# Performance work log

Measured on AMD Instinct MI355X. Metric: run time of the kernel, lower is better.

The kernel has to match this reference:

```python
import jax, jax.numpy as jnp
import numpy as np

THRESH = 0.5
DECAY = 0.2
D_IN = 784
H1 = 2048
H2 = 10
K = 10
U = D_IN + H1
L = 128
B = 1024


def setup_inputs() -> dict:
    key = jax.random.key(0)
    ks = jax.random.split(key, 6)
    inp = jax.random.uniform(ks[0], (B, D_IN), dtype=jnp.float32)
    W1 = jax.random.normal(ks[1], (H1, D_IN), dtype=jnp.float32) * 0.05
    b1 = jnp.zeros((H1,), dtype=jnp.float32)
    W2 = jax.random.normal(ks[2], (H2, H1), dtype=jnp.float32) * 0.05
    b2 = jnp.zeros((H2,), dtype=jnp.float32)
    # core_mem_all[k][u][0] -> sparse-ish per-unit vector, [1] -> count
    core_mem_vec = (jax.random.uniform(ks[3], (K, U, L)) > 0.7).astype(jnp.float32)
    core_mem_cnt = jax.random.randint(ks[4], (K, U), 0, 5).astype(jnp.int32)
    return {"input": inp, "W1": W1, "b1": b1, "W2": W2, "b2": b2,
            "core_mem_vec": core_mem_vec, "core_mem_cnt": core_mem_cnt,
            "time_window": 20}


def act_fun(mem):
    # spike = Heaviside(mem - thresh)
    return (mem > THRESH).astype(mem.dtype)


def reference(input, W1, b1, W2, b2, core_mem_vec, core_mem_cnt, time_window):
    batch, d_in = input.shape
    h1 = W1.shape[0]
    h2 = W2.shape[0]
    Lv = core_mem_vec.shape[-1]

    # Precompute, per (core k, unit u): contribution to count_add_1 / count_add_2
    # when unit u spikes. count_add_1 += (last nonzero index of temp) - 1 when cnt>0;
    # count_add_2 += cnt when cnt>0. Sum over cores up front (loop order irrelevant).
    nz = core_mem_vec != 0                                     # [K,U,L]
    has = nz.any(-1)
    last_idx = Lv - 1 - jnp.argmax(nz[..., ::-1].astype(jnp.int32), axis=-1)  # [K,U]
    active = (core_mem_cnt > 0) & has
    val1 = jnp.where(active, last_idx - 1, 0).sum(0).astype(jnp.float32)      # [U]
    val2 = jnp.where(core_mem_cnt > 0, core_mem_cnt, 0).sum(0).astype(jnp.float32)
    v1x, v1h = val1[:d_in], val1[d_in:]
    v2x, v2h = val2[:d_in], val2[d_in:]

    key = jax.random.key(42)

    def step(carry, t):
        h1m, h1s, h2m, h2s, h2sum, a1, a2, cs = carry
        # Bernoulli rate encoding of the input image
        x = (input > jax.random.uniform(jax.random.fold_in(key, t), input.shape)).astype(jnp.float32)
        # mem_update: mem = mem*decay*(1-spike) + W x + b ; spike = mem > thresh
        h1m = h1m * DECAY * (1.0 - h1s) + x @ W1.T + b1
        h1s = act_fun(h1m)
        h2m = h2m * DECAY * (1.0 - h2s) + h1s @ W2.T + b2
        h2s = act_fun(h2m)
        h2sum = h2sum + h2s
        # vectorized core-memory gather/count: sum per-unit precomputed values
        # over all spiking units, across the batch
        xs = x.sum(0)      # [784] spike counts per input unit this step
        hs = h1s.sum(0)    # [h1]
        a1 = a1 + xs @ v1x + hs @ v1h
        a2 = a2 + xs @ v2x + hs @ v2h
        cs = cs + xs.sum() + hs.sum()
        return (h1m, h1s, h2m, h2s, h2sum, a1, a2, cs), None

    z1 = jnp.zeros((batch, h1), dtype=jnp.float32)
    z2 = jnp.zeros((batch, h2), dtype=jnp.float32)
    carry = (z1, z1, z2, z2, z2, jnp.float32(0), jnp.float32(0), jnp.float32(0))
    carry, _ = jax.lax.scan(step, carry, jnp.arange(time_window))
    _, _, _, _, h2sum, a1, a2, cs = carry
    outputs = h2sum / time_window
    return outputs, a1, a2, cs
```

## Files before the change

### kernel.cpp

```cpp
#include <hip/hip_runtime.h>
#include <cstdint>
#include <cstddef>

static constexpr int D_IN = 784;
static constexpr int H1   = 2048;
static constexpr int H2   = 10;
static constexpr int KK   = 10;
static constexpr int UU   = 2832;
static constexpr int LL   = 128;
static constexpr int BB   = 1024;
static constexpr int TT   = 20;
static constexpr int HALF = BB * D_IN / 2;
static constexpr int NCH  = 25;
static constexpr int NLIMB = 3;
static constexpr int XA_T  = 32 * NCH * 64;
static constexpr int BITS_T = BB * 64;
static constexpr int PANEL = NCH * NLIMB * 64;
static constexpr int NPART_GEN = 2000;
static constexpr int NPART_H1  = 256;
static constexpr int NPART = NPART_GEN + NPART_H1;

static constexpr int BLK_VALS  = UU / 4;
static constexpr int BLK_W2T   = H1 / 256;
static constexpr int BLK_LIMBS = (64 * NCH * 64) / 256;
static constexpr int BLK_TRANS = D_IN * 4;
static constexpr int SETUP_BLOCKS = BLK_VALS + BLK_W2T + BLK_LIMBS + BLK_TRANS;

typedef int v4i  __attribute__((ext_vector_type(4)));
typedef int v16i __attribute__((ext_vector_type(16)));

#define MFMA_I8 __builtin_amdgcn_mfma_i32_32x32x32_i8

__device__ __forceinline__ uint32_t rotl32(uint32_t x, int d) {
  return (x << d) | (x >> (32 - d));
}
__device__ __forceinline__ void threefry2x32(uint32_t k0, uint32_t k1,
                                             uint32_t& x0, uint32_t& x1) {
  uint32_t ks2 = k0 ^ k1 ^ 0x1BD11BDAu;
  x0 += k0; x1 += k1;
#define TF_R(r) { x0 += x1; x1 = rotl32(x1, (r)); x1 ^= x0; }
  TF_R(13) TF_R(15) TF_R(26) TF_R(6)
  x0 += k1;  x1 += ks2 + 1u;
  TF_R(17) TF_R(29) TF_R(16) TF_R(24)
  x0 += ks2; x1 += k0 + 2u;
  TF_R(13) TF_R(15) TF_R(26) TF_R(6)
  x0 += k0;  x1 += k1 + 3u;
  TF_R(17) TF_R(29) TF_R(16) TF_R(24)
  x0 += k1;  x1 += ks2 + 4u;
  TF_R(13) TF_R(15) TF_R(26) TF_R(6)
  x0 += ks2; x1 += k0 + 5u;
#undef TF_R
}
__device__ __forceinline__ float bits_to_unif(uint32_t b) {
  uint32_t fb = (b >> 9) | 0x3F800000u;
  return __uint_as_float(fb) - 1.0f;
}

__device__ __forceinline__ double wave_red(double v) {
  #pragma unroll
  for (int off = 32; off > 0; off >>= 1) v += __shfl_down(v, off, 64);
  return v;
}
__device__ __forceinline__ void block_store3(double s0, double s1, double s2,
                                             double* slot) {
  __shared__ double lds[3][8];
  int lane = threadIdx.x & 63, w = threadIdx.x >> 6;
  int nw = (int)(blockDim.x >> 6);
  s0 = wave_red(s0); s1 = wave_red(s1); s2 = wave_red(s2);
  if (lane == 0) { lds[0][w] = s0; lds[1][w] = s1; lds[2][w] = s2; }
  __syncthreads();
  if (threadIdx.x == 0) {
    double t0 = 0, t1 = 0, t2 = 0;
    for (int i = 0; i < nw; i++) { t0 += lds[0][i]; t1 += lds[1][i]; t2 += lds[2][i]; }
    slot[0] = t0; slot[1] = t1; slot[2] = t2;
  }
}

__global__ __launch_bounds__(256)
void setup(const float* __restrict__ cmv, const int* __restrict__ cmc,
           float* __restrict__ v1, float* __restrict__ v2,
           const float* __restrict__ W2, float* __restrict__ W2T,
           const float* __restrict__ W1, v4i* __restrict__ W1L,
           const float* __restrict__ input, float* __restrict__ inT) {
  int bx = blockIdx.x;
  if (bx < BLK_VALS) {
    int u = bx * 4 + (threadIdx.x >> 6);
    int lane = threadIdx.x & 63;
    float acc1 = 0.0f, acc2 = 0.0f;
    for (int k = 0; k < KK; k++) {
      const float* p = cmv + ((size_t)k * UU + u) * LL;
      float a = p[lane];
      float b = p[lane + 64];
      unsigned long long mlo = __ballot(a != 0.0f);
      unsigned long long mhi = __ballot(b != 0.0f);
      int c = cmc[k * UU + u];
      if (c > 0) {
        int last = mhi ? (127 - __builtin_clzll(mhi))
                       : (mlo ? (63 - __builtin_clzll(mlo)) : -1);
        if (last >= 0) acc1 += (float)(last - 1);
        acc2 += (float)c;
      }
    }
    if (lane == 0) { v1[u] = acc1; v2[u] = acc2; }
  } else if (bx < BLK_VALS + BLK_W2T) {
    int i = (bx - BLK_VALS) * 256 + threadIdx.x;
    #pragma unroll
    for (int j = 0; j < H2; j++) W2T[i * H2 + j] = W2[j * H1 + i];
  } else if (bx < BLK_VALS + BLK_W2T + BLK_LIMBS) {
    int tid = (bx - BLK_VALS - BLK_W2T) * 256 + threadIdx.x;
    int lane = tid & 63;
    int tc = tid >> 6;
    int n = ((tc / NCH) << 5) + (lane & 31);
    int chunk = tc % NCH;
    int k0 = chunk * 32 + (lane >> 5) * 16;
    union { v4i v; signed char b[16]; } d[NLIMB];
    #pragma unroll
    for (int j = 0; j < 16; j++) {
      long long F = 0;
      int k = k0 + j;
      if (k < D_IN) {
        double w = (double)W1[(size_t)n * D_IN + k];
        F = llround(w * 0x1p24);
        if (F >  8355711LL) F =  8355711LL;
        if (F < -8421504LL) F = -8421504LL;
      }
      #pragma unroll
      for (int l = 0; l < NLIMB; l++) {
        int dig = (int)((F + 128) & 255) - 128;
        d[l].b[j] = (signed char)dig;
        F = (F - dig) >> 8;
      }
    }
    #pragma unroll
    for (int l = 0; l < NLIMB; l++) W1L[(size_t)(tc * NLIMB + l) * 64 + lane] = d[l].v;
  } else {
    int b = bx - (BLK_VALS + BLK_W2T + BLK_LIMBS);
    int k = b >> 2;
    int m = ((b & 3) << 8) + threadIdx.x;
    inT[(size_t)k * BB + m] = input[(size_t)m * D_IN + k];
  }
}

__global__ __launch_bounds__(256)
void gen_all(const float* __restrict__ inT, v4i* __restrict__ XA,
             const float* __restrict__ v1, const float* __restrict__ v2,
             double* __restrict__ gpart) {
  int t  = blockIdx.x / 100;
  int gw = (blockIdx.x % 100) * 4 + (threadIdx.x >> 6);
  int lane = threadIdx.x & 63;
  int mtile = gw / NCH, chunk = gw - mtile * NCH;
  int m = (mtile << 5) + (lane & 31);
  int k0 = chunk * 32 + (lane >> 5) * 16;
  uint32_t f0 = 0u, f1 = (uint32_t)t;
  threefry2x32(0u, 42u, f0, f1);
  union { v4i v; unsigned char b[16]; } r0, r1;
  double s0 = 0, s1 = 0, s2 = 0;
  v4i* XA_t = XA + (size_t)t * XA_T;
  if (k0 < D_IN) {
    #pragma unroll
    for (int j = 0; j < 16; j++) {
      int k = k0 + j;
      uint32_t c0 = (uint32_t)(m * D_IN + k), c1 = c0 + (uint32_t)HALF;
      threefry2x32(f0, f1, c0, c1);
      float u0 = bits_to_unif(c0), u1 = bits_to_unif(c1);
      float i0 = inT[(size_t)k * BB + m];
      float i1 = inT[(size_t)k * BB + m + 512];
      unsigned char x0 = (i0 > u0) ? 1 : 0;
      unsigned char x1 = (i1 > u1) ? 1 : 0;
      r0.b[j] = x0; r1.b[j] = x1;
      double xsum = (double)(x0 + x1);
      s0 += xsum * (double)v1[k];
      s1 += xsum * (double)v2[k];
      s2 += xsum;
    }
  } else {
    r0.v = (v4i){0, 0, 0, 0};
    r1.v = (v4i){0, 0, 0, 0};
  }
  XA_t[(size_t)(mtile * NCH + chunk) * 64 + lane] = r0.v;
  XA_t[(size_t)((mtile + 16) * NCH + chunk) * 64 + lane] = r1.v;
  block_store3(s0, s1, s2, gpart + 3 * (size_t)blockIdx.x);
}

__global__ __launch_bounds__(512, 2)
void h1_all(const v4i* __restrict__ XA, const v4i* __restrict__ W1L,
            const float* __restrict__ b1, uint32_t* __restrict__ bits,
            const float* __restrict__ v1, const float* __restrict__ v2,
            double* __restrict__ gpart) {
  extern __shared__ v4i bl[];
  int lane = threadIdx.x & 63, wv = threadIdx.x >> 6;
  int id = blockIdx.x + (blockIdx.y << 6);
  int xcd = id & 7;
  int idx = id >> 3;
  int ntile = (idx << 1) | (xcd >> 2);
  int mtg = xcd & 3;
  int mt = mtg * 8 + wv;
  {
    const v4i* wp = W1L + (size_t)ntile * PANEL;
    for (int i = threadIdx.x; i < PANEL; i += 512) bl[i] = wp[i];
  }
  __syncthreads();

  int col = lane & 31;
  int gn = (ntile << 5) + col;
  float bias = b1[gn];
  double v1n = (double)v1[D_IN + gn], v2n = (double)v2[D_IN + gn];
  int scnt = 0;
  float mreg[16];
  #pragma unroll
  for (int r = 0; r < 16; r++) mreg[r] = 0.0f;

  const v4i* bq = bl + lane;
  v4i B00 = bq[0],   B01 = bq[64],  B02 = bq[128];
  v4i B10 = bq[192], B11 = bq[256], B12 = bq[320];
  const v4i* a0 = XA + (size_t)mt * (NCH * 64) + lane;
  const v4i* a1 = a0 + XA_T;
  v4i A00 = a0[0], A10 = a1[0], A01 = a0[64], A11 = a1[64];

  #pragma unroll 1
  for (int tp = 0; tp < TT / 2; tp++) {
    v16i c00 = {}, c01 = {}, c02 = {};
    v16i c10 = {}, c11 = {}, c12 = {};
    __builtin_amdgcn_s_setprio(1);
    c00 = MFMA_I8(A00, B00, c00, 0, 0, 0);
    c10 = MFMA_I8(A10, B00, c10, 0, 0, 0);
    c01 = MFMA_I8(A00, B01, c01, 0, 0, 0);
    c11 = MFMA_I8(A10, B01, c11, 0, 0, 0);
    c02 = MFMA_I8(A00, B02, c02, 0, 0, 0);
    c12 = MFMA_I8(A10, B02, c12, 0, 0, 0);
    c00 = MFMA_I8(A01, B10, c00, 0, 0, 0);
    c10 = MFMA_I8(A11, B10, c10, 0, 0, 0);
    c01 = MFMA_I8(A01, B11, c01, 0, 0, 0);
    c11 = MFMA_I8(A11, B11, c11, 0, 0, 0);
    c02 = MFMA_I8(A01, B12, c02, 0, 0, 0);
    c12 = MFMA_I8(A11, B12, c12, 0, 0, 0);
    #pragma unroll
    for (int c = 2; c < NCH; c++) {
      v4i A0 = a0[c * 64], A1 = a1[c * 64];
      const v4i* br = bq + (size_t)c * (NLIMB * 64);
      v4i B0 = br[0], B1 = br[64], B2 = br[128];
      c00 = MFMA_I8(A0, B0, c00, 0, 0, 0);
      c10 = MFMA_I8(A1, B0, c10, 0, 0, 0);
      c01 = MFMA_I8(A0, B1, c01, 0, 0, 0);
      c11 = MFMA_I8(A1, B1, c11, 0, 0, 0);
      c02 = MFMA_I8(A0, B2, c02, 0, 0, 0);
      c12 = MFMA_I8(A1, B2, c12, 0, 0, 0);
    }
    __builtin_amdgcn_s_setprio(0);
    {
      const v4i* a0n = a0 + ((tp + 1 < TT / 2) ? 2 * XA_T : 0);
      const v4i* a1n = a0n + XA_T;
      A00 = a0n[0]; A10 = a1n[0]; A01 = a0n[64]; A11 = a1n[64];
      a0 = a0n; a1 = a1n;
    }
    #pragma unroll
    for (int half = 0; half < 2; half++) {
      const v16i& q0 = half ? c10 : c00;
      const v16i& q1 = half ? c11 : c01;
      const v16i& q2 = half ? c12 : c02;
      uint32_t* btm = bits + (size_t)(2 * tp + half) * BITS_T
                    + ((size_t)mt << 5) * 64 + ntile;
      #pragma unroll
      for (int r = 0; r < 16; r++) {
        int val = (int)((uint32_t)q0[r] + ((uint32_t)q1[r] << 8)
                        + ((uint32_t)q2[r] << 16));
        float dot = (float)val * 0x1p-24f + bias;
        float mp = mreg[r];
        float mnew = (mp > 0.5f) ? dot : fmaf(mp, 0.2f, dot);
        bool s = (mnew > 0.5f);
        mreg[r] = mnew;
        unsigned long long bm = __ballot(s);
        int rowA = (r & 3) + 8 * (r >> 2);
        if ((lane & 31) == 0)
          btm[(size_t)(rowA + ((lane >> 5) << 2)) * 64] = (uint32_t)(bm >> (lane & 32));
        scnt += s ? 1 : 0;
      }
    }
  }
  double sc = (double)scnt;
  block_store3(sc * v1n, sc * v2n, sc, gpart + 3 * (size_t)(NPART_GEN + id));
}

__global__ __launch_bounds__(256)
void h2_all(const uint32_t* __restrict__ bits, const float* __restrict__ W2T,
            const float* __restrict__ b2, const double* __restrict__ gpart,
            float* __restrict__ out) {
  int lane = threadIdx.x & 63, wq = threadIdx.x >> 6;
  int b0 = blockIdx.x * 2;
  float w[8][10];
  #pragma unroll
  for (int c = 0; c < 8; c++) {
    int n = (wq << 9) + (c << 6) + lane;
    #pragma unroll
    for (int j = 0; j < 10; j++) w[c][j] = W2T[(size_t)n * H2 + j];
  }
  float m = 0.0f, sp = 0.0f, sm = 0.0f;
  float b2v = (lane < 10) ? b2[lane] : 0.0f;
  __shared__ float part[4][2][10];
  #pragma unroll 1
  for (int t = 0; t < TT; t++) {
    const uint32_t* bt = bits + (size_t)t * BITS_T;
    #pragma unroll
    for (int r = 0; r < 2; r++) {
      uint32_t myw = bt[(size_t)(b0 + r) * 64 + (wq << 4) + (lane & 15)];
      float p[10];
      #pragma unroll
      for (int j = 0; j < 10; j++) p[j] = 0.0f;
      #pragma unroll
      for (int c = 0; c < 8; c++) {
        uint32_t wd = __shfl(myw, (c << 1) + (lane >> 5), 64);
        float f = (float)((wd >> (lane & 31)) & 1u);
        #pragma unroll
        for (int j = 0; j < 10; j++) p[j] += f * w[c][j];
      }
      #pragma unroll
      for (int j = 0; j < 10; j++) {
        float v = p[j];
        #pragma unroll
        for (int off = 32; off > 0; off >>= 1) v += __shfl_xor(v, off, 64);
        p[j] = v;
      }
      if (lane == 0) {
        #pragma unroll
        for (int j = 0; j < 10; j++) part[wq][r][j] = p[j];
      }
    }
    __syncthreads();
    if (wq < 2 && lane < 10) {
      float red = part[0][wq][lane] + part[1][wq][lane]
                + part[2][wq][lane] + part[3][wq][lane];
      m = m * 0.2f * (1.0f - sp) + red + b2v;
      sp = (m > 0.5f) ? 1.0f : 0.0f;
      sm += sp;
    }
    __syncthreads();
  }
  if (wq < 2 && lane < 10)
    out[(size_t)(b0 + wq) * H2 + lane] = (float)((double)sm / (double)TT);

  if (blockIdx.x == 0) {
    double t0 = 0, t1 = 0, t2 = 0;
    for (int i = threadIdx.x; i < NPART; i += 256) {
      t0 += gpart[3 * (size_t)i];
      t1 += gpart[3 * (size_t)i + 1];
      t2 += gpart[3 * (size_t)i + 2];
    }
    __shared__ double fin[3][4];
    t0 = wave_red(t0); t1 = wave_red(t1); t2 = wave_red(t2);
    if (lane == 0) { fin[0][wq] = t0; fin[1][wq] = t1; fin[2][wq] = t2; }
    __syncthreads();
    if (threadIdx.x == 0) {
      double a = 0, b = 0, cc = 0;
      #pragma unroll
      for (int i = 0; i < 4; i++) { a += fin[0][i]; b += fin[1][i]; cc += fin[2][i]; }
      out[(size_t)BB * H2 + 0] = (float)a;
      out[(size_t)BB * H2 + 1] = (float)b;
      out[(size_t)BB * H2 + 2] = (float)cc;
    }
  }
}

extern "C" void kernel_launch(void* const* d_in, const int* in_sizes, int n_in,
                              void* d_out, int out_size, void* d_ws, size_t ws_size,
                              hipStream_t stream) {
  (void)in_sizes; (void)n_in; (void)out_size; (void)ws_size;
  const float* input = (const float*)d_in[0];
  const float* W1    = (const float*)d_in[1];
  const float* b1    = (const float*)d_in[2];
  const float* W2    = (const float*)d_in[3];
  const float* b2    = (const float*)d_in[4];
  const float* cmv   = (const float*)d_in[5];
  const int*   cmc   = (const int*)d_in[6];

  char* base = (char*)d_ws;
  float*  v1   = (float*)(base + 0);
  float*  v2   = (float*)(base + 11328);
  float*  W2T  = (float*)(base + 22656);
  v4i*    W1L  = (v4i*)(base + 104576);
  v4i*    XA   = (v4i*)(base + 5019776);
  uint32_t* bits = (uint32_t*)(base + 21403776);
  float*  inT  = (float*)(base + 26646656);
  double* gpart = (double*)(base + 29857920);

  setup<<<SETUP_BLOCKS, 256, 0, stream>>>(cmv, cmc, v1, v2, W2, W2T, W1, W1L,
                                          input, inT);
  gen_all<<<TT * 100, 256, 0, stream>>>(inT, XA, v1, v2, gpart);
  h1_all<<<dim3(64, 4), 512, PANEL * 16, stream>>>(XA, W1L, b1, bits, v1, v2,
                                                   gpart);
  h2_all<<<BB / 2, 256, 0, stream>>>(bits, W2T, b2, gpart, (float*)d_out);
}
```

Measured before the change: 285.8 us.

## Fuse all four stages into one cooperative persistent kernel with grid syncs

Replaces the four separate launches (setup, Bernoulli generation, int8-MFMA hidden layer, output layer) with one cooperative kernel of 256 blocks of 512 threads, separated by grid-wide barriers. Each block handles two virtual 256-thread blocks in the setup and generation phases. This removes launch gaps and kernel-boundary drains. The h1 phase also preloads a third B/A chunk and staggers odd waves with s_sleep, and the h2 phase is remapped to 4 rows per block. The cost is that the setup and generation phases now run on only 256 resident blocks, and grid.sync adds barrier overhead.

```diff
diff --git a/kernel.cpp b/kernel.cpp
--- a/kernel.cpp
+++ b/kernel.cpp
@@ -1,4 +1,5 @@
 #include <hip/hip_runtime.h>
+#include <hip/hip_cooperative_groups.h>
 #include <cstdint>
 #include <cstddef>
 
@@ -25,6 +26,7 @@
 static constexpr int BLK_LIMBS = (64 * NCH * 64) / 256;
 static constexpr int BLK_TRANS = D_IN * 4;
 static constexpr int SETUP_BLOCKS = BLK_VALS + BLK_W2T + BLK_LIMBS + BLK_TRANS;
+static constexpr int BLK_GEN   = TT * 100;
 
 typedef int v4i  __attribute__((ext_vector_type(4)));
 typedef int v16i __attribute__((ext_vector_type(16)));
@@ -61,301 +63,340 @@
   for (int off = 32; off > 0; off >>= 1) v += __shfl_down(v, off, 64);
   return v;
 }
+__device__ __forceinline__ void half_store3(double s0, double s1, double s2,
+                                            double* slot, bool act) {
+  __shared__ double hl[2][3][4];
+  int h = threadIdx.x >> 8, lane = threadIdx.x & 63, w = (threadIdx.x >> 6) & 3;
+  s0 = wave_red(s0); s1 = wave_red(s1); s2 = wave_red(s2);
+  if (lane == 0) { hl[h][0][w] = s0; hl[h][1][w] = s1; hl[h][2][w] = s2; }
+  __syncthreads();
+  if ((threadIdx.x & 255) == 0 && act) {
+    double t0 = 0, t1 = 0, t2 = 0;
+    #pragma unroll
+    for (int i = 0; i < 4; i++) { t0 += hl[h][0][i]; t1 += hl[h][1][i]; t2 += hl[h][2][i]; }
+    slot[0] = t0; slot[1] = t1; slot[2] = t2;
+  }
+  __syncthreads();
+}
 __device__ __forceinline__ void block_store3(double s0, double s1, double s2,
                                              double* slot) {
   __shared__ double lds[3][8];
   int lane = threadIdx.x & 63, w = threadIdx.x >> 6;
-  int nw = (int)(blockDim.x >> 6);
   s0 = wave_red(s0); s1 = wave_red(s1); s2 = wave_red(s2);
   if (lane == 0) { lds[0][w] = s0; lds[1][w] = s1; lds[2][w] = s2; }
   __syncthreads();
   if (threadIdx.x == 0) {
     double t0 = 0, t1 = 0, t2 = 0;
-    for (int i = 0; i < nw; i++) { t0 += lds[0][i]; t1 += lds[1][i]; t2 += lds[2][i]; }
+    #pragma unroll
+    for (int i = 0; i < 8; i++) { t0 += lds[0][i]; t1 += lds[1][i]; t2 += lds[2][i]; }
     slot[0] = t0; slot[1] = t1; slot[2] = t2;
   }
 }
 
-__global__ __launch_bounds__(256)
-void setup(const float* __restrict__ cmv, const int* __restrict__ cmc,
-           float* __restrict__ v1, float* __restrict__ v2,
-           const float* __restrict__ W2, float* __restrict__ W2T,
-           const float* __restrict__ W1, v4i* __restrict__ W1L,
-           const float* __restrict__ input, float* __restrict__ inT) {
-  int bx = blockIdx.x;
-  if (bx < BLK_VALS) {
-    int u = bx * 4 + (threadIdx.x >> 6);
-    int lane = threadIdx.x & 63;
-    float acc1 = 0.0f, acc2 = 0.0f;
-    for (int k = 0; k < KK; k++) {
-      const float* p = cmv + ((size_t)k * UU + u) * LL;
-      float a = p[lane];
-      float b = p[lane + 64];
-      unsigned long long mlo = __ballot(a != 0.0f);
-      unsigned long long mhi = __ballot(b != 0.0f);
-      int c = cmc[k * UU + u];
-      if (c > 0) {
-        int last = mhi ? (127 - __builtin_clzll(mhi))
-                       : (mlo ? (63 - __builtin_clzll(mlo)) : -1);
-        if (last >= 0) acc1 += (float)(last - 1);
-        acc2 += (float)c;
-      }
-    }
-    if (lane == 0) { v1[u] = acc1; v2[u] = acc2; }
-  } else if (bx < BLK_VALS + BLK_W2T) {
-    int i = (bx - BLK_VALS) * 256 + threadIdx.x;
+__global__ __launch_bounds__(512, 2)
+void scnn_all(const float* __restrict__ cmv, const int* __restrict__ cmc,
+              float* __restrict__ v1, float* __restrict__ v2,
+              const float* __restrict__ W2, float* __restrict__ W2T,
+              const float* __restrict__ W1, v4i* __restrict__ W1L,
+              const float* __restrict__ input, float* __restrict__ inT,
+              v4i* __restrict__ XA, const float* __restrict__ b1,
+              uint32_t* __restrict__ bits, double* __restrict__ gpart,
+              const float* __restrict__ b2, float* __restrict__ out) {
+  namespace cg = cooperative_groups;
+  cg::grid_group grid = cg::this_grid();
+  extern __shared__ v4i bl[];
+  int tid = threadIdx.x, bid = blockIdx.x;
+
+  for (int it = 0; it < (SETUP_BLOCKS + 511) / 512; ++it) {
+    int vb = it * 512 + bid * 2 + (tid >> 8);
+    int vt = tid & 255;
+    if (vb >= SETUP_BLOCKS) continue;
+    if (vb < BLK_VALS) {
+      int u = vb * 4 + (vt >> 6);
+      int lane = vt & 63;
+      float acc1 = 0.0f, acc2 = 0.0f;
+      for (int k = 0; k < KK; k++) {
+        const float* p = cmv + ((size_t)k * UU + u) * LL;
+        float a = p[lane];
+        float b = p[lane + 64];
+        unsigned long long mlo = __ballot(a != 0.0f);
+        unsigned long long mhi = __ballot(b != 0.0f);
+        int c = cmc[k * UU + u];
+        if (c > 0) {
+          int last = mhi ? (127 - __builtin_clzll(mhi))
+                         : (mlo ? (63 - __builtin_clzll(mlo)) : -1);
+          if (last >= 0) acc1 += (float)(last - 1);
+          acc2 += (float)c;
+        }
+      }
+      if (lane == 0) { v1[u] = acc1; v2[u] = acc2; }
+    } else if (vb < BLK_VALS + BLK_W2T) {
+      int i = (vb - BLK_VALS) * 256 + vt;
+      #pragma unroll
+      for (int j = 0; j < H2; j++) W2T[i * H2 + j] = W2[j * H1 + i];
+    } else if (vb < BLK_VALS + BLK_W2T + BLK_LIMBS) {
+      int tl = (vb - BLK_VALS - BLK_W2T) * 256 + vt;
+      int lane = tl & 63;
+      int tc = tl >> 6;
+      int n = ((tc / NCH) << 5) + (lane & 31);
+      int chunk = tc % NCH;
+      int k0 = chunk * 32 + (lane >> 5) * 16;
+      union { v4i v; signed char b[16]; } d[NLIMB];
+      #pragma unroll
+      for (int j = 0; j < 16; j++) {
+        long long F = 0;
+        int k = k0 + j;
+        if (k < D_IN) {
+          double w = (double)W1[(size_t)n * D_IN + k];
+          F = llround(w * 0x1p24);
+          if (F >  8355711LL) F =  8355711LL;
+          if (F < -8421504LL) F = -8421504LL;
+        }
+        #pragma unroll
+        for (int l = 0; l < NLIMB; l++) {
+          int dig = (int)((F + 128) & 255) - 128;
+          d[l].b[j] = (signed char)dig;
+          F = (F - dig) >> 8;
+        }
+      }
+      #pragma unroll
+      for (int l = 0; l < NLIMB; l++) W1L[(size_t)(tc * NLIMB + l) * 64 + lane] = d[l].v;
+    } else {
+      int b = vb - (BLK_VALS + BLK_W2T + BLK_LIMBS);
+      int k = b >> 2;
+      int m = ((b & 3) << 8) + vt;
+      inT[(size_t)k * BB + m] = input[(size_t)m * D_IN + k];
+    }
+  }
+  grid.sync();
+
+  for (int it = 0; it < (BLK_GEN + 511) / 512; ++it) {
+    int vb = it * 512 + bid * 2 + (tid >> 8);
+    int vt = tid & 255;
+    bool act = (vb < BLK_GEN);
+    double s0 = 0, s1 = 0, s2 = 0;
+    if (act) {
+      int lane = vt & 63;
+      int t = vb / 100;
+      int gw = (vb % 100) * 4 + (vt >> 6);
+      int mtile = gw / NCH, chunk = gw - mtile * NCH;
+      int m = (mtile << 5) + (lane & 31);
+      int k0 = chunk * 32 + (lane >> 5) * 16;
+      uint32_t f0 = 0u, f1 = (uint32_t)t;
+      threefry2x32(0u, 42u, f0, f1);
+      union { v4i v; unsigned char b[16]; } r0, r1;
+      v4i* XA_t = XA + (size_t)t * XA_T;
+      if (k0 < D_IN) {
+        #pragma unroll
+        for (int j = 0; j < 16; j++) {
+          int k = k0 + j;
+          uint32_t c0 = (uint32_t)(m * D_IN + k), c1 = c0 + (uint32_t)HALF;
+          threefry2x32(f0, f1, c0, c1);
+          float u0 = bits_to_unif(c0), u1 = bits_to_unif(c1);
+          float i0 = inT[(size_t)k * BB + m];
+          float i1 = inT[(size_t)k * BB + m + 512];
+          unsigned char x0 = (i0 > u0) ? 1 : 0;
+          unsigned char x1 = (i1 > u1) ? 1 : 0;
+          r0.b[j] = x0; r1.b[j] = x1;
+          double xsum = (double)(x0 + x1);
+          s0 += xsum * (double)v1[k];
+          s1 += xsum * (double)v2[k];
+          s2 += xsum;
+        }
+      } else {
+        r0.v = (v4i){0, 0, 0, 0};
+        r1.v = (v4i){0, 0, 0, 0};
+      }
+      XA_t[(size_t)(mtile * NCH + chunk) * 64 + lane] = r0.v;
+      XA_t[(size_t)((mtile + 16) * NCH + chunk) * 64 + lane] = r1.v;
+    }
+    half_store3(s0, s1, s2, gpart + 3 * (size_t)(act ? vb : 0), act);
+  }
+  grid.sync();
+
+  {
+    int lane = tid & 63, wv = tid >> 6;
+    int id = bid;
+    int xcd = id & 7;
+    int idx = id >> 3;
+    int ntile = (idx << 1) | (xcd >> 2);
+    int mtg = xcd & 3;
+    int mt = mtg * 8 + wv;
+    {
+      const v4i* wp = W1L + (size_t)ntile * PANEL;
+      for (int i = tid; i < PANEL; i += 512) bl[i] = wp[i];
+    }
+    __syncthreads();
+
+    int col = lane & 31;
+    int gn = (ntile << 5) + col;
+    float bias = b1[gn];
+    double v1n = (double)v1[D_IN + gn], v2n = (double)v2[D_IN + gn];
+    int scnt = 0;
+    float mreg[16];
     #pragma unroll
-    for (int j = 0; j < H2; j++) W2T[i * H2 + j] = W2[j * H1 + i];
-  } else if (bx < BLK_VALS + BLK_W2T + BLK_LIMBS) {
-    int tid = (bx - BLK_VALS - BLK_W2T) * 256 + threadIdx.x;
-    int lane = tid & 63;
-    int tc = tid >> 6;
-    int n = ((tc / NCH) << 5) + (lane & 31);
-    int chunk = tc % NCH;
-    int k0 = chunk * 32 + (lane >> 5) * 16;
-    union { v4i v; signed char b[16]; } d[NLIMB];
+    for (int r = 0; r < 16; r++) mreg[r] = 0.0f;
+
+    const v4i* bq = bl + lane;
+    v4i B00 = bq[0],   B01 = bq[64],  B02 = bq[128];
+    v4i B10 = bq[192], B11 = bq[256], B12 = bq[320];
+    v4i B20 = bq[384], B21 = bq[448], B22 = bq[512];
+    const v4i* a0 = XA + (size_t)mt * (NCH * 64) + lane;
+    const v4i* a1 = a0 + XA_T;
+    v4i A00 = a0[0], A10 = a1[0], A01 = a0[64], A11 = a1[64];
+    v4i A02 = a0[128], A12 = a1[128];
+
+    if (wv & 1) __builtin_amdgcn_s_sleep(104);
+
+    #pragma unroll 1
+    for (int tp = 0; tp < TT / 2; tp++) {
+      v16i c00 = {}, c01 = {}, c02 = {};
+      v16i c10 = {}, c11 = {}, c12 = {};
+      __builtin_amdgcn_s_setprio(1);
+      c00 = MFMA_I8(A00, B00, c00, 0, 0, 0);
+      c10 = MFMA_I8(A10, B00, c10, 0, 0, 0);
+      c01 = MFMA_I8(A00, B01, c01, 0, 0, 0);
+      c11 = MFMA_I8(A10, B01, c11, 0, 0, 0);
+      c02 = MFMA_I8(A00, B02, c02, 0, 0, 0);
+      c12 = MFMA_I8(A10, B02, c12, 0, 0, 0);
+      c00 = MFMA_I8(A01, B10, c00, 0, 0, 0);
+      c10 = MFMA_I8(A11, B10, c10, 0, 0, 0);
+      c01 = MFMA_I8(A01, B11, c01, 0, 0, 0);
+      c11 = MFMA_I8(A11, B11, c11, 0, 0, 0);
+      c02 = MFMA_I8(A01, B12, c02, 0, 0, 0);
+      c12 = MFMA_I8(A11, B12, c12, 0, 0, 0);
+      c00 = MFMA_I8(A02, B20, c00, 0, 0, 0);
+      c10 = MFMA_I8(A12, B20, c10, 0, 0, 0);
+      c01 = MFMA_I8(A02, B21, c01, 0, 0, 0);
+      c11 = MFMA_I8(A12, B21, c11, 0, 0, 0);
+      c02 = MFMA_I8(A02, B22, c02, 0, 0, 0);
+      c12 = MFMA_I8(A12, B22, c12, 0, 0, 0);
+      #pragma unroll
+      for (int c = 3; c < NCH; c++) {
+        v4i A0 = a0[c * 64], A1 = a1[c * 64];
+        const v4i* br = bq + (size_t)c * (NLIMB * 64);
+        v4i B0 = br[0], B1 = br[64], B2 = br[128];
+        c00 = MFMA_I8(A0, B0, c00, 0, 0, 0);
+        c10 = MFMA_I8(A1, B0, c10, 0, 0, 0);
+        c01 = MFMA_I8(A0, B1, c01, 0, 0, 0);
+        c11 = MFMA_I8(A1, B1, c11, 0, 0, 0);
+        c02 = MFMA_I8(A0, B2, c02, 0, 0, 0);
+        c12 = MFMA_I8(A1, B2, c12, 0, 0, 0);
+      }
+      __builtin_amdgcn_s_setprio(0);
+      {
+        const v4i* a0n = a0 + ((tp + 1 < TT / 2) ? 2 * XA_T : 0);
+        const v4i* a1n = a0n + XA_T;
+        A00 = a0n[0]; A10 = a1n[0]; A01 = a0n[64]; A11 = a1n[64];
+        A02 = a0n[128]; A12 = a1n[128];
+        a0 = a0n; a1 = a1n;
+      }
+      #pragma unroll
+      for (int half = 0; half < 2; half++) {
+        const v16i& q0 = half ? c10 : c00;
+        const v16i& q1 = half ? c11 : c01;
+        const v16i& q2 = half ? c12 : c02;
+        uint32_t* btm = bits + (size_t)(2 * tp + half) * BITS_T
+                      + ((size_t)mt << 5) * 64 + ntile;
+        #pragma unroll
+        for (int r = 0; r < 16; r++) {
+          int val = (int)((uint32_t)q0[r] + ((uint32_t)q1[r] << 8)
+                          + ((uint32_t)q2[r] << 16));
+          float dot = (float)val * 0x1p-24f + bias;
+          float mp = mreg[r];
+          float mnew = (mp > 0.5f) ? dot : fmaf(mp, 0.2f, dot);
+          bool s = (mnew > 0.5f);
+          mreg[r] = mnew;
+          unsigned long long bm = __ballot(s);
+          int rowA = (r & 3) + 8 * (r >> 2);
+          if ((lane & 31) == 0)
+            btm[(size_t)(rowA + ((lane >> 5) << 2)) * 64] = (uint32_t)(bm >> (lane & 32));
+          scnt += s ? 1 : 0;
+        }
+      }
+    }
+    double sc = (double)scnt;
+    block_store3(sc * v1n, sc * v2n, sc, gpart + 3 * (size_t)(NPART_GEN + id));
+  }
+  grid.sync();
+
+  {
+    int lane = tid & 63, wq = tid >> 6;
+    int whalf = wq >> 2, q = wq & 3;
+    int b0 = bid * 4;
+    int joff = (lane & 32) ? 5 : 0;
+    float w[16][5];
     #pragma unroll
-    for (int j = 0; j < 16; j++) {
-      long long F = 0;
-      int k = k0 + j;
-      if (k < D_IN) {
-        double w = (double)W1[(size_t)n * D_IN + k];
-        F = llround(w * 0x1p24);
-        if (F >  8355711LL) F =  8355711LL;
-        if (F < -8421504LL) F = -8421504LL;
-      }
-      #pragma unroll
-      for (int l = 0; l < NLIMB; l++) {
-        int dig = (int)((F + 128) & 255) - 128;
-        d[l].b[j] = (signed char)dig;
-        F = (F - dig) >> 8;
-      }
-    }
-    #pragma unroll
-    for (int l = 0; l < NLIMB; l++) W1L[(size_t)(tc * NLIMB + l) * 64 + lane] = d[l].v;
-  } else {
-    int b = bx - (BLK_VALS + BLK_W2T + BLK_LIMBS);
-    int k = b >> 2;
-    int m = ((b & 3) << 8) + threadIdx.x;
-    inT[(size_t)k * BB + m] = input[(size_t)m * D_IN + k];
-  }
-}
-
-__global__ __launch_bounds__(256)
-void gen_all(const float* __restrict__ inT, v4i* __restrict__ XA,
-             const float* __restrict__ v1, const float* __restrict__ v2,
-             double* __restrict__ gpart) {
-  int t  = blockIdx.x / 100;
-  int gw = (blockIdx.x % 100) * 4 + (threadIdx.x >> 6);
-  int lane = threadIdx.x & 63;
-  int mtile = gw / NCH, chunk = gw - mtile * NCH;
-  int m = (mtile << 5) + (lane & 31);
-  int k0 = chunk * 32 + (lane >> 5) * 16;
-  uint32_t f0 = 0u, f1 = (uint32_t)t;
-  threefry2x32(0u, 42u, f0, f1);
-  union { v4i v; unsigned char b[16]; } r0, r1;
-  double s0 = 0, s1 = 0, s2 = 0;
-  v4i* XA_t = XA + (size_t)t * XA_T;
-  if (k0 < D_IN) {
-    #pragma unroll
-    for (int j = 0; j < 16; j++) {
-      int k = k0 + j;
-      uint32_t c0 = (uint32_t)(m * D_IN + k), c1 = c0 + (uint32_t)HALF;
-      threefry2x32(f0, f1, c0, c1);
-      float u0 = bits_to_unif(c0), u1 = bits_to_unif(c1);
-      float i0 = inT[(size_t)k * BB + m];
-      float i1 = inT[(size_t)k * BB + m + 512];
-      unsigned char x0 = (i0 > u0) ? 1 : 0;
-      unsigned char x1 = (i1 > u1) ? 1 : 0;
-      r0.b[j] = x0; r1.b[j] = x1;
-      double xsum = (double)(x0 + x1);
-      s0 += xsum * (double)v1[k];
-      s1 += xsum * (double)v2[k];
-      s2 += xsum;
-    }
-  } else {
-    r0.v = (v4i){0, 0, 0, 0};
-    r1.v = (v4i){0, 0, 0, 0};
-  }
-  XA_t[(size_t)(mtile * NCH + chunk) * 64 + lane] = r0.v;
-  XA_t[(size_t)((mtile + 16) * NCH + chunk) * 64 + lane] = r1.v;
-  block_store3(s0, s1, s2, gpart + 3 * (size_t)blockIdx.x);
-}
-
-__global__ __launch_bounds__(512, 2)
-void h1_all(const v4i* __restrict__ XA, const v4i* __restrict__ W1L,
-            const float* __restrict__ b1, uint32_t* __restrict__ bits,
-            const float* __restrict__ v1, const float* __restrict__ v2,
-            double* __restrict__ gpart) {
-  extern __shared__ v4i bl[];
-  int lane = threadIdx.x & 63, wv = threadIdx.x >> 6;
-  int id = blockIdx.x + (blockIdx.y << 6);
-  int xcd = id & 7;
-  int idx = id >> 3;
-  int ntile = (idx << 1) | (xcd >> 2);
-  int mtg = xcd & 3;
-  int mt = mtg * 8 + wv;
-  {
-    const v4i* wp = W1L + (size_t)ntile * PANEL;
-    for (int i = threadIdx.x; i < PANEL; i += 512) bl[i] = wp[i];
-  }
-  __syncthreads();
-
-  int col = lane & 31;
-  int gn = (ntile << 5) + col;
-  float bias = b1[gn];
-  double v1n = (double)v1[D_IN + gn], v2n = (double)v2[D_IN + gn];
-  int scnt = 0;
-  float mreg[16];
-  #pragma unroll
-  for (int r = 0; r < 16; r++) mreg[r] = 0.0f;
-
-  const v4i* bq = bl + lane;
-  v4i B00 = bq[0],   B01 = bq[64],  B02 = bq[128];
-  v4i B10 = bq[192], B11 = bq[256], B12 = bq[320];
-  const v4i* a0 = XA + (size_t)mt * (NCH * 64) + lane;
-  const v4i* a1 = a0 + XA_T;
-  v4i A00 = a0[0], A10 = a1[0], A01 = a0[64], A11 = a1[64];
-
-  #pragma unroll 1
-  for (int tp = 0; tp < TT / 2; tp++) {
-    v16i c00 = {}, c01 = {}, c02 = {};
-    v16i c10 = {}, c11 = {}, c12 = {};
-    __builtin_amdgcn_s_setprio(1);
-    c00 = MFMA_I8(A00, B00, c00, 0, 0, 0);
-    c10 = MFMA_I8(A10, B00, c10, 0, 0, 0);
-    c01 = MFMA_I8(A00, B01, c01, 0, 0, 0);
-    c11 = MFMA_I8(A10, B01, c11, 0, 0, 0);
-    c02 = MFMA_I8(A00, B02, c02, 0, 0, 0);
-    c12 = MFMA_I8(A10, B02, c12, 0, 0, 0);
-    c00 = MFMA_I8(A01, B10, c00, 0, 0, 0);
-    c10 = MFMA_I8(A11, B10, c10, 0, 0, 0);
-    c01 = MFMA_I8(A01, B11, c01, 0, 0, 0);
-    c11 = MFMA_I8(A11, B11, c11, 0, 0, 0);
-    c02 = MFMA_I8(A01, B12, c02, 0, 0, 0);
-    c12 = MFMA_I8(A11, B12, c12, 0, 0, 0);
-    #pragma unroll
-    for (int c = 2; c < NCH; c++) {
-      v4i A0 = a0[c * 64], A1 = a1[c * 64];
-      const v4i* br = bq + (size_t)c * (NLIMB * 64);
-      v4i B0 = br[0], B1 = br[64], B2 = br[128];
-      c00 = MFMA_I8(A0, B0, c00, 0, 0, 0);
-      c10 = MFMA_I8(A1, B0, c10, 0, 0, 0);
-      c01 = MFMA_I8(A0, B1, c01, 0, 0, 0);
-      c11 = MFMA_I8(A1, B1, c11, 0, 0, 0);
-      c02 = MFMA_I8(A0, B2, c02, 0, 0, 0);
-      c12 = MFMA_I8(A1, B2, c12, 0, 0, 0);
-    }
-    __builtin_amdgcn_s_setprio(0);
-    {
-      const v4i* a0n = a0 + ((tp + 1 < TT / 2) ? 2 * XA_T : 0);
-      const v4i* a1n = a0n + XA_T;
-      A00 = a0n[0]; A10 = a1n[0]; A01 = a0n[64]; A11 = a1n[64];
-      a0 = a0n; a1 = a1n;
-    }
-    #pragma unroll
-    for (int half = 0; half < 2; half++) {
-      const v16i& q0 = half ? c10 : c00;
-      const v16i& q1 = half ? c11 : c01;
-      const v16i& q2 = half ? c12 : c02;
-      uint32_t* btm = bits + (size_t)(2 * tp + half) * BITS_T
-                    + ((size_t)mt << 5) * 64 + ntile;
-      #pragma unroll
-      for (int r = 0; r < 16; r++) {
-        int val = (int)((uint32_t)q0[r] + ((uint32_t)q1[r] << 8)
-                        + ((uint32_t)q2[r] << 16));
-        float dot = (float)val * 0x1p-24f + bias;
-        float mp = mreg[r];
-        float mnew = (mp > 0.5f) ? dot : fmaf(mp, 0.2f, dot);
-        bool s = (mnew > 0.5f);
-        mreg[r] = mnew;
-        unsigned long long bm = __ballot(s);
-        int rowA = (r & 3) + 8 * (r >> 2);
-        if ((lane & 31) == 0)
-          btm[(size_t)(rowA + ((lane >> 5) << 2)) * 64] = (uint32_t)(bm >> (lane & 32));
-        scnt += s ? 1 : 0;
-      }
-    }
-  }
-  double sc = (double)scnt;
-  block_store3(sc * v1n, sc * v2n, sc, gpart + 3 * (size_t)(NPART_GEN + id));
-}
-
-__global__ __launch_bounds__(256)
-void h2_all(const uint32_t* __restrict__ bits, const float* __restrict__ W2T,
-            const float* __restrict__ b2, const double* __restrict__ gpart,
-            float* __restrict__ out) {
-  int lane = threadIdx.x & 63, wq = threadIdx.x >> 6;
-  int b0 = blockIdx.x * 2;
-  float w[8][10];
-  #pragma unroll
-  for (int c = 0; c < 8; c++) {
-    int n = (wq << 9) + (c << 6) + lane;
-    #pragma unroll
-    for (int j = 0; j < 10; j++) w[c][j] = W2T[(size_t)n * H2 + j];
-  }
-  float m = 0.0f, sp = 0.0f, sm = 0.0f;
-  float b2v = (lane < 10) ? b2[lane] : 0.0f;
-  __shared__ float part[4][2][10];
-  #pragma unroll 1
-  for (int t = 0; t < TT; t++) {
-    const uint32_t* bt = bits + (size_t)t * BITS_T;
-    #pragma unroll
-    for (int r = 0; r < 2; r++) {
-      uint32_t myw = bt[(size_t)(b0 + r) * 64 + (wq << 4) + (lane & 15)];
-      float p[10];
-      #pragma unroll
-      for (int j = 0; j < 10; j++) p[j] = 0.0f;
-      #pragma unroll
-      for (int c = 0; c < 8; c++) {
-        uint32_t wd = __shfl(myw, (c << 1) + (lane >> 5), 64);
-        float f = (float)((wd >> (lane & 31)) & 1u);
-        #pragma unroll
-        for (int j = 0; j < 10; j++) p[j] += f * w[c][j];
-      }
-      #pragma unroll
-      for (int j = 0; j < 10; j++) {
-        float v = p[j];
-        #pragma unroll
-        for (int off = 32; off > 0; off >>= 1) v += __shfl_xor(v, off, 64);
-        p[j] = v;
-      }
-      if (lane == 0) {
-        #pragma unroll
-        for (int j = 0; j < 10; j++) part[wq][r][j] = p[j];
-      }
-    }
-    __syncthreads();
-    if (wq < 2 && lane < 10) {
-      float red = part[0][wq][lane] + part[1][wq][lane]
-                + part[2][wq][lane] + part[3][wq][lane];
-      m = m * 0.2f * (1.0f - sp) + red + b2v;
-      sp = (m > 0.5f) ? 1.0f : 0.0f;
-      sm += sp;
-    }
-    __syncthreads();
-  }
-  if (wq < 2 && lane < 10)
-    out[(size_t)(b0 + wq) * H2 + lane] = (float)((double)sm / (double)TT);
-
-  if (blockIdx.x == 0) {
-    double t0 = 0, t1 = 0, t2 = 0;
-    for (int i = threadIdx.x; i < NPART; i += 256) {
-      t0 += gpart[3 * (size_t)i];
-      t1 += gpart[3 * (size_t)i + 1];
-      t2 += gpart[3 * (size_t)i + 2];
-    }
-    __shared__ double fin[3][4];
-    t0 = wave_red(t0); t1 = wave_red(t1); t2 = wave_red(t2);
-    if (lane == 0) { fin[0][wq] = t0; fin[1][wq] = t1; fin[2][wq] = t2; }
-    __syncthreads();
-    if (threadIdx.x == 0) {
-      double a = 0, b = 0, cc = 0;
-      #pragma unroll
-      for (int i = 0; i < 4; i++) { a += fin[0][i]; b += fin[1][i]; cc += fin[2][i]; }
-      out[(size_t)BB * H2 + 0] = (float)a;
-      out[(size_t)BB * H2 + 1] = (float)b;
-      out[(size_t)BB * H2 + 2] = (float)cc;
+    for (int c = 0; c < 16; c++) {
+      int n = (q << 9) + (c << 5) + (lane & 31);
+      #pragma unroll
+      for (int jj = 0; jj < 5; jj++) w[c][jj] = W2T[(size_t)n * H2 + joff + jj];
+    }
+    float m = 0.0f, sp = 0.0f, sm = 0.0f;
+    float b2v = (lane < 10) ? b2[lane] : 0.0f;
+    __shared__ float part2[2][4][2][10];
+    #pragma unroll 1
+    for (int t = 0; t < TT; t++) {
+      const uint32_t* bt = bits + (size_t)t * BITS_T;
+      #pragma unroll
+      for (int r = 0; r < 2; r++) {
+        int row = b0 + whalf * 2 + r;
+        uint32_t myw = bt[(size_t)row * 64 + (q << 4) + (lane & 15)];
+        float p[5];
+        #pragma unroll
+        for (int jj = 0; jj < 5; jj++) p[jj] = 0.0f;
+        #pragma unroll
+        for (int c = 0; c < 16; c++) {
+          uint32_t wd = __shfl(myw, c, 64);
+          float f = (float)((wd >> (lane & 31)) & 1u);
+          #pragma unroll
+          for (int jj = 0; jj < 5; jj++) p[jj] += f * w[c][jj];
+        }
+        #pragma unroll
+        for (int jj = 0; jj < 5; jj++) {
+          float v = p[jj];
+          #pragma unroll
+          for (int off = 16; off > 0; off >>= 1) v += __shfl_xor(v, off, 64);
+          p[jj] = v;
+        }
+        if ((lane & 31) == 0) {
+          #pragma unroll
+          for (int jj = 0; jj < 5; jj++) part2[whalf][q][r][joff + jj] = p[jj];
+        }
+      }
+      __syncthreads();
+      if (wq < 4 && lane < 10) {
+        float red = part2[wq >> 1][0][wq & 1][lane] + part2[wq >> 1][1][wq & 1][lane]
+                  + part2[wq >> 1][2][wq & 1][lane] + part2[wq >> 1][3][wq & 1][lane];
+        m = m * 0.2f * (1.0f - sp) + red + b2v;
+        sp = (m > 0.5f) ? 1.0f : 0.0f;
+        sm += sp;
+      }
+      __syncthreads();
+    }
+    if (wq < 4 && lane < 10)
+      out[(size_t)(b0 + wq) * H2 + lane] = (float)((double)sm / (double)TT);
+
+    if (bid == 0) {
+      double t0 = 0, t1 = 0, t2 = 0;
+      for (int i = tid; i < NPART; i += 512) {
+        t0 += gpart[3 * (size_t)i];
+        t1 += gpart[3 * (size_t)i + 1];
+        t2 += gpart[3 * (size_t)i + 2];
+      }
+      __shared__ double fin[3][8];
+      int w8 = tid >> 6;
+      t0 = wave_red(t0); t1 = wave_red(t1); t2 = wave_red(t2);
+      if (lane == 0) { fin[0][w8] = t0; fin[1][w8] = t1; fin[2][w8] = t2; }
+      __syncthreads();
+      if (tid == 0) {
+        double a = 0, b = 0, cc = 0;
+        #pragma unroll
+        for (int i = 0; i < 8; i++) { a += fin[0][i]; b += fin[1][i]; cc += fin[2][i]; }
+        out[(size_t)BB * H2 + 0] = (float)a;
+        out[(size_t)BB * H2 + 1] = (float)b;
+        out[(size_t)BB * H2 + 2] = (float)cc;
+      }
     }
   }
 }
@@ -364,13 +405,13 @@
                               void* d_out, int out_size, void* d_ws, size_t ws_size,
                               hipStream_t stream) {
   (void)in_sizes; (void)n_in; (void)out_size; (void)ws_size;
+  const float* cmv_i = (const float*)d_in[5];
+  const int*   cmc_i = (const int*)d_in[6];
   const float* input = (const float*)d_in[0];
   const float* W1    = (const float*)d_in[1];
   const float* b1    = (const float*)d_in[2];
   const float* W2    = (const float*)d_in[3];
   const float* b2    = (const float*)d_in[4];
-  const float* cmv   = (const float*)d_in[5];
-  const int*   cmc   = (const int*)d_in[6];
 
   char* base = (char*)d_ws;
   float*  v1   = (float*)(base + 0);
@@ -382,10 +423,13 @@
   float*  inT  = (float*)(base + 26646656);
   double* gpart = (double*)(base + 29857920);
 
-  setup<<<SETUP_BLOCKS, 256, 0, stream>>>(cmv, cmc, v1, v2, W2, W2T, W1, W1L,
-                                          input, inT);
-  gen_all<<<TT * 100, 256, 0, stream>>>(inT, XA, v1, v2, gpart);
-  h1_all<<<dim3(64, 4), 512, PANEL * 16, stream>>>(XA, W1L, b1, bits, v1, v2,
-                                                   gpart);
-  h2_all<<<BB / 2, 256, 0, stream>>>(bits, W2T, b2, gpart, (float*)d_out);
-}
+  float* outp = (float*)d_out;
+  void* args[] = {
+    (void*)&cmv_i, (void*)&cmc_i, (void*)&v1, (void*)&v2,
+    (void*)&W2, (void*)&W2T, (void*)&W1, (void*)&W1L,
+    (void*)&input, (void*)&inT, (void*)&XA, (void*)&b1,
+    (void*)&bits, (void*)&gpart, (void*)&b2, (void*)&outp
+  };
+  hipLaunchCooperativeKernel((const void*)scnn_all, dim3(256), dim3(512), args,
+                             (unsigned)(PANEL * 16), stream);
+}
```

Result: slower. 384.3 us (+34.5%).

## Tile input transpose via LDS, pack float2 pairs, software-pipeline h1 MFMA loads

Applied to the files above, without the earlier changes.

The input transpose in setup now runs through a shared-memory tile with float4 reads and float2-packed writes, so each gen_all thread fetches both batch halves with one load instead of two strided ones. The h1_all inner loop is rewritten as a rotating register pipeline: A fragments are prefetched three chunks ahead and B fragments two chunks ahead, including the next timestep's first chunks, so loads overlap the MFMAs. Odd waves sleep briefly at the start to stagger them against even waves. The cost is more live vector registers, which could pressure occupancy at the 512x2 launch bound.

```diff
diff --git a/kernel.cpp b/kernel.cpp
--- a/kernel.cpp
+++ b/kernel.cpp
@@ -23,7 +23,7 @@
 static constexpr int BLK_VALS  = UU / 4;
 static constexpr int BLK_W2T   = H1 / 256;
 static constexpr int BLK_LIMBS = (64 * NCH * 64) / 256;
-static constexpr int BLK_TRANS = D_IN * 4;
+static constexpr int BLK_TRANS = 16 * 13;
 static constexpr int SETUP_BLOCKS = BLK_VALS + BLK_W2T + BLK_LIMBS + BLK_TRANS;
 
 typedef int v4i  __attribute__((ext_vector_type(4)));
@@ -81,7 +81,7 @@
            float* __restrict__ v1, float* __restrict__ v2,
            const float* __restrict__ W2, float* __restrict__ W2T,
            const float* __restrict__ W1, v4i* __restrict__ W1L,
-           const float* __restrict__ input, float* __restrict__ inT) {
+           const float* __restrict__ input, float2* __restrict__ inT2) {
   int bx = blockIdx.x;
   if (bx < BLK_VALS) {
     int u = bx * 4 + (threadIdx.x >> 6);
@@ -134,15 +134,42 @@
     #pragma unroll
     for (int l = 0; l < NLIMB; l++) W1L[(size_t)(tc * NLIMB + l) * 64 + lane] = d[l].v;
   } else {
-    int b = bx - (BLK_VALS + BLK_W2T + BLK_LIMBS);
-    int k = b >> 2;
-    int m = ((b & 3) << 8) + threadIdx.x;
-    inT[(size_t)k * BB + m] = input[(size_t)m * D_IN + k];
+    int tile = bx - (BLK_VALS + BLK_W2T + BLK_LIMBS);
+    int tm = tile / 13, tk = tile % 13;
+    int mb = tm * 32, k0 = tk * 64;
+    int ncol = (tk == 12) ? 16 : 64;
+    __shared__ float ts[64][65];
+    int tid = threadIdx.x;
+    if (tk == 12) {
+      for (int idx = tid; idx < 64 * 4; idx += 256) {
+        int r = idx >> 2, c4 = idx & 3;
+        int m = mb + (r & 31) + ((r >> 5) << 9);
+        const float4* src = (const float4*)(input + (size_t)m * D_IN + k0 + c4 * 4);
+        float4 vq = *src;
+        ts[r][c4 * 4 + 0] = vq.x; ts[r][c4 * 4 + 1] = vq.y;
+        ts[r][c4 * 4 + 2] = vq.z; ts[r][c4 * 4 + 3] = vq.w;
+      }
+    } else {
+      for (int idx = tid; idx < 64 * 16; idx += 256) {
+        int r = idx >> 4, c4 = idx & 15;
+        int m = mb + (r & 31) + ((r >> 5) << 9);
+        const float4* src = (const float4*)(input + (size_t)m * D_IN + k0 + c4 * 4);
+        float4 vq = *src;
+        ts[r][c4 * 4 + 0] = vq.x; ts[r][c4 * 4 + 1] = vq.y;
+        ts[r][c4 * 4 + 2] = vq.z; ts[r][c4 * 4 + 3] = vq.w;
+      }
+    }
+    __syncthreads();
+    for (int idx = tid; idx < ncol * 32; idx += 256) {
+      int kr = idx >> 5, mc = idx & 31;
+      inT2[(size_t)(k0 + kr) * 512 + mb + mc] =
+          make_float2(ts[mc][kr], ts[32 + mc][kr]);
+    }
   }
 }
 
 __global__ __launch_bounds__(256)
-void gen_all(const float* __restrict__ inT, v4i* __restrict__ XA,
+void gen_all(const float2* __restrict__ inT2, v4i* __restrict__ XA,
              const float* __restrict__ v1, const float* __restrict__ v2,
              double* __restrict__ gpart) {
   int t  = blockIdx.x / 100;
@@ -163,10 +190,9 @@
       uint32_t c0 = (uint32_t)(m * D_IN + k), c1 = c0 + (uint32_t)HALF;
       threefry2x32(f0, f1, c0, c1);
       float u0 = bits_to_unif(c0), u1 = bits_to_unif(c1);
-      float i0 = inT[(size_t)k * BB + m];
-      float i1 = inT[(size_t)k * BB + m + 512];
-      unsigned char x0 = (i0 > u0) ? 1 : 0;
-      unsigned char x1 = (i1 > u1) ? 1 : 0;
+      float2 iv = inT2[(size_t)k * 512 + m];
+      unsigned char x0 = (iv.x > u0) ? 1 : 0;
+      unsigned char x1 = (iv.y > u1) ? 1 : 0;
       r0.b[j] = x0; r1.b[j] = x1;
       double xsum = (double)(x0 + x1);
       s0 += xsum * (double)v1[k];
@@ -211,48 +237,51 @@
   for (int r = 0; r < 16; r++) mreg[r] = 0.0f;
 
   const v4i* bq = bl + lane;
-  v4i B00 = bq[0],   B01 = bq[64],  B02 = bq[128];
-  v4i B10 = bq[192], B11 = bq[256], B12 = bq[320];
   const v4i* a0 = XA + (size_t)mt * (NCH * 64) + lane;
   const v4i* a1 = a0 + XA_T;
-  v4i A00 = a0[0], A10 = a1[0], A01 = a0[64], A11 = a1[64];
+  v4i Ab[3][2], Bb[2][3];
+  Ab[0][0] = a0[0];   Ab[0][1] = a1[0];
+  Ab[1][0] = a0[64];  Ab[1][1] = a1[64];
+  Ab[2][0] = a0[128]; Ab[2][1] = a1[128];
+  Bb[0][0] = bq[0];   Bb[0][1] = bq[64];  Bb[0][2] = bq[128];
+  Bb[1][0] = bq[192]; Bb[1][1] = bq[256]; Bb[1][2] = bq[320];
+
+  if (wv & 1) __builtin_amdgcn_s_sleep(96);
 
   #pragma unroll 1
   for (int tp = 0; tp < TT / 2; tp++) {
+    const v4i* a0n = (tp < TT / 2 - 1) ? (a0 + 2 * XA_T)
+                                       : (XA + (size_t)mt * (NCH * 64) + lane);
+    const v4i* a1n = a0n + XA_T;
     v16i c00 = {}, c01 = {}, c02 = {};
     v16i c10 = {}, c11 = {}, c12 = {};
     __builtin_amdgcn_s_setprio(1);
-    c00 = MFMA_I8(A00, B00, c00, 0, 0, 0);
-    c10 = MFMA_I8(A10, B00, c10, 0, 0, 0);
-    c01 = MFMA_I8(A00, B01, c01, 0, 0, 0);
-    c11 = MFMA_I8(A10, B01, c11, 0, 0, 0);
-    c02 = MFMA_I8(A00, B02, c02, 0, 0, 0);
-    c12 = MFMA_I8(A10, B02, c12, 0, 0, 0);
-    c00 = MFMA_I8(A01, B10, c00, 0, 0, 0);
-    c10 = MFMA_I8(A11, B10, c10, 0, 0, 0);
-    c01 = MFMA_I8(A01, B11, c01, 0, 0, 0);
-    c11 = MFMA_I8(A11, B11, c11, 0, 0, 0);
-    c02 = MFMA_I8(A01, B12, c02, 0, 0, 0);
-    c12 = MFMA_I8(A11, B12, c12, 0, 0, 0);
-    #pragma unroll
-    for (int c = 2; c < NCH; c++) {
-      v4i A0 = a0[c * 64], A1 = a1[c * 64];
-      const v4i* br = bq + (size_t)c * (NLIMB * 64);
-      v4i B0 = br[0], B1 = br[64], B2 = br[128];
+    #pragma unroll
+    for (int c = 0; c < NCH; c++) {
+      v4i A0 = Ab[c % 3][0], A1 = Ab[c % 3][1];
+      v4i B0 = Bb[c % 2][0], B1 = Bb[c % 2][1], B2 = Bb[c % 2][2];
       c00 = MFMA_I8(A0, B0, c00, 0, 0, 0);
       c10 = MFMA_I8(A1, B0, c10, 0, 0, 0);
       c01 = MFMA_I8(A0, B1, c01, 0, 0, 0);
       c11 = MFMA_I8(A1, B1, c11, 0, 0, 0);
       c02 = MFMA_I8(A0, B2, c02, 0, 0, 0);
       c12 = MFMA_I8(A1, B2, c12, 0, 0, 0);
+      if (c <= 21) {
+        Ab[c % 3][0] = a0[(c + 3) * 64];
+        Ab[c % 3][1] = a1[(c + 3) * 64];
+      } else {
+        const int nc = (c == 24) ? 0 : (c - 21);
+        Ab[c % 3][0] = a0n[nc * 64];
+        Ab[c % 3][1] = a1n[nc * 64];
+      }
+      {
+        const int bc = (c <= 22) ? (c + 2) : ((c == 23) ? 1 : 0);
+        const v4i* br = bq + (size_t)bc * (NLIMB * 64);
+        Bb[c % 2][0] = br[0]; Bb[c % 2][1] = br[64]; Bb[c % 2][2] = br[128];
+      }
     }
     __builtin_amdgcn_s_setprio(0);
-    {
-      const v4i* a0n = a0 + ((tp + 1 < TT / 2) ? 2 * XA_T : 0);
-      const v4i* a1n = a0n + XA_T;
-      A00 = a0n[0]; A10 = a1n[0]; A01 = a0n[64]; A11 = a1n[64];
-      a0 = a0n; a1 = a1n;
-    }
+    a0 = a0n; a1 = a1n;
     #pragma unroll
     for (int half = 0; half < 2; half++) {
       const v16i& q0 = half ? c10 : c00;
@@ -379,12 +408,12 @@
   v4i*    W1L  = (v4i*)(base + 104576);
   v4i*    XA   = (v4i*)(base + 5019776);
   uint32_t* bits = (uint32_t*)(base + 21403776);
-  float*  inT  = (float*)(base + 26646656);
+  float2* inT2 = (float2*)(base + 26646656);
   double* gpart = (double*)(base + 29857920);
 
   setup<<<SETUP_BLOCKS, 256, 0, stream>>>(cmv, cmc, v1, v2, W2, W2T, W1, W1L,
-                                          input, inT);
-  gen_all<<<TT * 100, 256, 0, stream>>>(inT, XA, v1, v2, gpart);
+                                          input, inT2);
+  gen_all<<<TT * 100, 256, 0, stream>>>(inT2, XA, v1, v2, gpart);
   h1_all<<<dim3(64, 4), 512, PANEL * 16, stream>>>(XA, W1L, b1, bits, v1, v2,
                                                    gpart);
   h2_all<<<BB / 2, 256, 0, stream>>>(bits, W2T, b2, gpart, (float*)d_out);
```

New measurement: 288.3 us. No clear change (+0.9%).
